# Kernel optimization log

Hardware: AMD Instinct MI355X
Metric: run time of the kernel (lower is better)

Reference implementation:

```python
import jax, jax.numpy as jnp
import numpy as np
from jax import lax

BETA = 1e-07
LAMBDA_TV = 1e-08


def _resize_bilinear_ac(x, out_h, out_w):
    """Bilinear resize with align_corners=True, NCHW layout (matches F.interpolate)."""
    B, C, H, W = x.shape
    ys = jnp.arange(out_h, dtype=jnp.float32) * ((H - 1) / max(out_h - 1, 1))
    xs = jnp.arange(out_w, dtype=jnp.float32) * ((W - 1) / max(out_w - 1, 1))
    y0 = jnp.floor(ys).astype(jnp.int32); y1 = jnp.minimum(y0 + 1, H - 1)
    x0 = jnp.floor(xs).astype(jnp.int32); x1 = jnp.minimum(x0 + 1, W - 1)
    wy = (ys - y0.astype(jnp.float32))[:, None]   # [out_h,1]
    wx = (xs - x0.astype(jnp.float32))[None, :]   # [1,out_w]
    r0 = x[:, :, y0, :]; r1 = x[:, :, y1, :]      # [B,C,out_h,W]
    top = r0[:, :, :, x0] * (1.0 - wx) + r0[:, :, :, x1] * wx
    bot = r1[:, :, :, x0] * (1.0 - wx) + r1[:, :, :, x1] * wx
    return top * (1.0 - wy) + bot * wy


def _levelset_loss(output, target):
    B = output.shape[0]
    # pcentroid computed under no_grad in torch -> stop_gradient here
    num = jnp.einsum('bthw,bchw->btc', target, output)
    den = jnp.sum(output, axis=(2, 3))                       # [B,C]
    pcent = lax.stop_gradient(num / den[:, None, :])          # [B,T,C]
    plevel = target[:, :, None, :, :] - pcent[:, :, :, None, None]  # [B,T,C,H,W]
    return jnp.sum(plevel * plevel * output[:, None]) / B


def _gradient_loss2d(output):
    B = output.shape[0]
    dH = jnp.abs(output[:, :, 1:, :] - output[:, :, :-1, :])
    dW = jnp.abs(output[:, :, :, 1:] - output[:, :, :, :-1])
    return (jnp.sum(dH) + jnp.sum(dW)) / B


def _nonlocal_tv_loss(f_output, f_sem):
    B, Cs, H, W = f_sem.shape
    N = H * W
    fo = _resize_bilinear_ac(f_output, H, W)                  # [B,C,H,W]
    C = fo.shape[1]
    # F.normalize(f_sem, dim=1) (eps=1e-12)
    norm = jnp.sqrt(jnp.sum(f_sem * f_sem, axis=1, keepdims=True))
    sem = f_sem / jnp.maximum(norm, 1e-12)
    sem_f = sem.reshape(B, Cs, N)
    # tau[b,r,p] = relu(<sem_r, sem_p>); normalized by global spatial max per (b,r)
    tau = jax.nn.relu(jnp.einsum('bcr,bcp->brp', sem_f, sem_f))  # [B,N,N]
    tau_max = jnp.max(tau, axis=2, keepdims=True)
    tau_n = tau / (tau_max + 1e-05)
    # torch.matmul(dL[B,C,H,W], tau[B,1,H,W]) summed over everything reduces to
    # sum_{i,k,j} dL[b,c,i,k] * tau[b,k,j] = sum_k (sum_i dL[b,c,i,k]) * (sum_j tau[b,k,j])
    t = tau_n.reshape(B, N, H, W).sum(axis=3)                 # [B,N,H] row-sums of tau
    of = fo.reshape(B, C, N)
    # dL[b,c,r,h,w] = |out_r - out_{(h,w)}| (penalty='l1')
    dL = jnp.abs(of[:, :, :, None, None] - fo[:, :, None, :, :])  # [B,C,N,H,W]
    A = dL.sum(axis=3)                                         # [B,C,N,W] sum over rows i
    return jnp.einsum('bcrk,brk->', A, t) / B


def setup_inputs() -> dict:
    key = jax.random.key(0)
    k1, k2, k3, k4 = jax.random.split(key, 4)
    return {
        'output': jax.random.uniform(k1, (4, 21, 512, 512), dtype=jnp.float32),
        'target': jax.random.uniform(k2, (4, 3, 512, 512), dtype=jnp.float32),
        'f_sem': jax.random.normal(k3, (4, 256, 32, 32), dtype=jnp.float32),
        'f_output': jax.random.uniform(k4, (4, 21, 64, 64), dtype=jnp.float32),
        'use_NonLocal_TV': 1,
    }


def reference(output, target, f_sem, f_output, use_NonLocal_TV):
    loss_LS = _levelset_loss(output, target)
    if use_NonLocal_TV:
        loss_TV = _nonlocal_tv_loss(f_output, f_sem) * LAMBDA_TV
    else:
        loss_TV = _gradient_loss2d(output) * LAMBDA_TV
    loss_MS = (loss_LS + loss_TV) * BETA
    return (loss_LS * BETA, loss_TV * BETA, loss_MS)
```

## Files before the change

kernel.cpp:

```cpp
#include <hip/hip_runtime.h>

#define BETA_F   1e-7f
#define LAMBDA_F 1e-8f

#define HWSZ 262144
#define NBC  84
#define NPIX 1024

#define OFF_FO    0
#define OFF_GSUM  86016
#define OFF_INVN  (86016 + 131072)
#define OFF_RMAX  (217088 + 4096)
#define OFF_LS    (221184 + 4096)
#define OFF_ACC   (225280 + 588)
#define ZERO_START OFF_RMAX
#define ZERO_COUNT (4096 + 588 + 4)

#define N_GRAM_BLK 144

typedef __attribute__((ext_vector_type(8))) short short8;
typedef __attribute__((ext_vector_type(4))) float f32x4;

__device__ const unsigned char RT_[36] =
    {0,0,0,0,0,0,0,0, 1,1,1,1,1,1,1, 2,2,2,2,2,2, 3,3,3,3,3, 4,4,4,4, 5,5,5, 6,6, 7};
__device__ const unsigned char CT_[36] =
    {0,1,2,3,4,5,6,7, 1,2,3,4,5,6,7, 2,3,4,5,6,7, 3,4,5,6,7, 4,5,6,7, 5,6,7, 6,7, 7};

__device__ __forceinline__ unsigned short bf16r(float f) {
    unsigned int u = __float_as_uint(f);
    u += 0x7fffu + ((u >> 16) & 1u);
    return (unsigned short)(u >> 16);
}

__global__ __launch_bounds__(256) void k_prep(const float* __restrict__ fo_in,
                                              const float* __restrict__ fsem,
                                              float* __restrict__ ws) {
    const int bid = blockIdx.x, tid = threadIdx.x;
    if (bid < 19) {
        int i = bid * 256 + tid;
        if (i < ZERO_COUNT) ws[ZERO_START + i] = 0.f;
    } else if (bid < 103) {
        const int bc = bid - 19;
        const float* im = fo_in + bc * 4096;
        for (int p = tid; p < 1024; p += 256) {
            const int oy = p >> 5, ox = p & 31;
            const float R = 63.0f / 31.0f;
            float sy = oy * R, sx = ox * R;
            int y0 = (int)sy, x0 = (int)sx;
            int y1 = min(y0 + 1, 63), x1 = min(x0 + 1, 63);
            float wy = sy - (float)y0, wx = sx - (float)x0;
            float v00 = im[y0 * 64 + x0], v01 = im[y0 * 64 + x1];
            float v10 = im[y1 * 64 + x0], v11 = im[y1 * 64 + x1];
            float top = v00 * (1.f - wx) + v01 * wx;
            float bot = v10 * (1.f - wx) + v11 * wx;
            ws[OFF_FO + bc * NPIX + p] = top * (1.f - wy) + bot * wy;
        }
    } else {
        const int blk = bid - 103;
        const int b = blk >> 4, pg = blk & 15;
        const int p0 = pg * 64;
        const int pi = tid & 63, cg = tid >> 6;
        float s = 0.f;
        for (int c = cg; c < 256; c += 4) {
            float v = fsem[(b * 256 + c) * 1024 + p0 + pi];
            s += v * v;
        }
        __shared__ float red[4][64];
        red[cg][pi] = s;
        __syncthreads();
        if (tid < 64) {
            float t = red[0][tid] + red[1][tid] + red[2][tid] + red[3][tid];
            ws[OFF_INVN + b * 1024 + p0 + tid] = 1.f / fmaxf(sqrtf(t), 1e-12f);
        }
    }
}

__device__ __forceinline__ void acc_px(float4 o, float4 ta, float4 tb, float4 tc,
                                       float& dn, float& n0, float& n1, float& n2,
                                       float& q0, float& q1, float& q2) {
    dn += o.x + o.y + o.z + o.w;
    n0 += ta.x*o.x + ta.y*o.y + ta.z*o.z + ta.w*o.w;
    q0 += ta.x*ta.x*o.x + ta.y*ta.y*o.y + ta.z*ta.z*o.z + ta.w*ta.w*o.w;
    n1 += tb.x*o.x + tb.y*o.y + tb.z*o.z + tb.w*o.w;
    q1 += tb.x*tb.x*o.x + tb.y*tb.y*o.y + tb.z*tb.z*o.z + tb.w*tb.w*o.w;
    n2 += tc.x*o.x + tc.y*o.y + tc.z*o.z + tc.w*o.w;
    q2 += tc.x*tc.x*o.x + tc.y*tc.y*o.y + tc.z*tc.z*o.z + tc.w*tc.w*o.w;
}

#define LSTR 40

__global__ __launch_bounds__(256) void k_main(const float* __restrict__ outp,
                                              const float* __restrict__ tgt,
                                              const float* __restrict__ fsem,
                                              float* __restrict__ ws) {
    __shared__ __align__(16) char smem[20480];
    const int tid = threadIdx.x;

    if (blockIdx.x < N_GRAM_BLK) {
        unsigned short* Asub = (unsigned short*)smem;
        unsigned short* Bsub = (unsigned short*)(smem + 10240);
        const int bid = blockIdx.x;
        const int b = bid / 36, t = bid % 36;
        const int rt = RT_[t], ct = CT_[t];
        const bool diag = (rt == ct);
        const int r0 = rt * 128, c0 = ct * 128;

        const int ch_l = tid & 31, pxg = tid >> 5;
        const int w = tid >> 6, l = tid & 63;
        const int wr = (w >> 1) * 64, wc = (w & 1) * 64;
        const int lr = l & 15, lg = l >> 4;

        f32x4 acc[4][4];
        #pragma unroll
        for (int i = 0; i < 4; ++i)
            #pragma unroll
            for (int j = 0; j < 4; ++j) acc[i][j] = (f32x4){0.f, 0.f, 0.f, 0.f};

        for (int kk = 0; kk < 8; ++kk) {
            __syncthreads();
            const float* fb = fsem + (size_t)(b * 256 + kk * 32 + ch_l) * 1024;
            #pragma unroll
            for (int q = 0; q < 4; ++q) {
                float4 va = *(const float4*)(fb + r0 + pxg * 16 + q * 4);
                float4 vb = *(const float4*)(fb + c0 + pxg * 16 + q * 4);
                const int px = pxg * 16 + q * 4;
                Asub[(px + 0) * LSTR + ch_l] = bf16r(va.x);
                Asub[(px + 1) * LSTR + ch_l] = bf16r(va.y);
                Asub[(px + 2) * LSTR + ch_l] = bf16r(va.z);
                Asub[(px + 3) * LSTR + ch_l] = bf16r(va.w);
                Bsub[(px + 0) * LSTR + ch_l] = bf16r(vb.x);
                Bsub[(px + 1) * LSTR + ch_l] = bf16r(vb.y);
                Bsub[(px + 2) * LSTR + ch_l] = bf16r(vb.z);
                Bsub[(px + 3) * LSTR + ch_l] = bf16r(vb.w);
            }
            __syncthreads();
            short8 a8[4], b8[4];
            #pragma unroll
            for (int fr = 0; fr < 4; ++fr)
                a8[fr] = *(const short8*)(Asub + (wr + fr * 16 + lr) * LSTR + lg * 8);
            #pragma unroll
            for (int fc = 0; fc < 4; ++fc)
                b8[fc] = *(const short8*)(Bsub + (wc + fc * 16 + lr) * LSTR + lg * 8);
            #pragma unroll
            for (int fr = 0; fr < 4; ++fr)
                #pragma unroll
                for (int fc = 0; fc < 4; ++fc)
                    acc[fr][fc] = __builtin_amdgcn_mfma_f32_16x16x32_bf16(
                        a8[fr], b8[fc], acc[fr][fc], 0, 0, 0);
        }

        float ir[4][4], ic[4];
        #pragma unroll
        for (int fr = 0; fr < 4; ++fr)
            #pragma unroll
            for (int rg = 0; rg < 4; ++rg)
                ir[fr][rg] = ws[OFF_INVN + b * 1024 + r0 + wr + fr * 16 + lg * 4 + rg];
        #pragma unroll
        for (int fc = 0; fc < 4; ++fc)
            ic[fc] = ws[OFF_INVN + b * 1024 + c0 + wc + fc * 16 + lr];
        #pragma unroll
        for (int fr = 0; fr < 4; ++fr)
            #pragma unroll
            for (int fc = 0; fc < 4; ++fc)
                #pragma unroll
                for (int rg = 0; rg < 4; ++rg)
                    acc[fr][fc][rg] = fmaxf(acc[fr][fc][rg], 0.f) * ir[fr][rg] * ic[fc];

        #pragma unroll
        for (int fr = 0; fr < 4; ++fr)
            #pragma unroll
            for (int rg = 0; rg < 4; ++rg) {
                float v0 = acc[fr][0][rg] + acc[fr][1][rg];
                float v1 = acc[fr][2][rg] + acc[fr][3][rg];
                float m  = fmaxf(fmaxf(acc[fr][0][rg], acc[fr][1][rg]),
                                 fmaxf(acc[fr][2][rg], acc[fr][3][rg]));
                #pragma unroll
                for (int msk = 1; msk < 16; msk <<= 1) {
                    v0 += __shfl_xor(v0, msk);
                    v1 += __shfl_xor(v1, msk);
                    m = fmaxf(m, __shfl_xor(m, msk));
                }
                if (lr == 0) {
                    const int row = r0 + wr + fr * 16 + lg * 4 + rg;
                    float* g = ws + OFF_GSUM + (size_t)(b * 1024 + row) * 32
                             + ct * 4 + (w & 1) * 2;
                    g[0] = v0; g[1] = v1;
                    atomicMax((int*)&ws[OFF_RMAX + b * 1024 + row], __float_as_int(m));
                }
            }
        if (!diag) {
            #pragma unroll
            for (int fc = 0; fc < 4; ++fc) {
                float c0s = 0.f, c1s = 0.f, cm = 0.f;
                #pragma unroll
                for (int rg = 0; rg < 4; ++rg) {
                    c0s += acc[0][fc][rg] + acc[1][fc][rg];
                    c1s += acc[2][fc][rg] + acc[3][fc][rg];
                    cm = fmaxf(cm, fmaxf(fmaxf(acc[0][fc][rg], acc[1][fc][rg]),
                                         fmaxf(acc[2][fc][rg], acc[3][fc][rg])));
                }
                #pragma unroll
                for (int msk = 16; msk < 64; msk <<= 1) {
                    c0s += __shfl_xor(c0s, msk);
                    c1s += __shfl_xor(c1s, msk);
                    cm = fmaxf(cm, __shfl_xor(cm, msk));
                }
                if (lg == 0) {
                    const int col = c0 + wc + fc * 16 + lr;
                    float* g = ws + OFF_GSUM + (size_t)(b * 1024 + col) * 32
                             + rt * 4 + (w >> 1) * 2;
                    g[0] = c0s; g[1] = c1s;
                    atomicMax((int*)&ws[OFF_RMAX + b * 1024 + col], __float_as_int(cm));
                }
            }
        }
    } else {
        float (*red)[7] = (float (*)[7])smem;
        const int blk = blockIdx.x - N_GRAM_BLK;
        const int slice = blk & 31, bc = blk >> 5;
        const int b = bc / 21;
        const float4* o4 = (const float4*)(outp + (size_t)bc * HWSZ + slice * 8192);
        const float4* t4 = (const float4*)(tgt + (size_t)b * (3 * HWSZ) + slice * 8192);
        float dn = 0, n0 = 0, n1 = 0, n2 = 0, q0 = 0, q1 = 0, q2 = 0;
        #pragma unroll
        for (int half = 0; half < 2; ++half) {
            float4 o[4], ta[4], tb[4], tc[4];
            #pragma unroll
            for (int j = 0; j < 4; ++j) {
                const int i = tid + (half * 4 + j) * 256;
                o[j]  = o4[i];
                ta[j] = t4[i];
                tb[j] = t4[i + 65536];
                tc[j] = t4[i + 131072];
            }
            #pragma unroll
            for (int j = 0; j < 4; ++j)
                acc_px(o[j], ta[j], tb[j], tc[j], dn, n0, n1, n2, q0, q1, q2);
        }
        float vals[7] = {n0, n1, n2, q0, q1, q2, dn};
        #pragma unroll
        for (int j = 0; j < 7; ++j) {
            float v = vals[j];
            #pragma unroll
            for (int off = 32; off; off >>= 1) v += __shfl_xor(v, off);
            if ((tid & 63) == 0) red[tid >> 6][j] = v;
        }
        __syncthreads();
        if (tid < 7) {
            float s = red[0][tid] + red[1][tid] + red[2][tid] + red[3][tid];
            atomicAdd(&ws[OFF_LS + bc * 7 + tid], s);
        }
    }
}

__global__ __launch_bounds__(256) void k_tv(const float* __restrict__ ws,
                                            float* __restrict__ acc_out) {
    const int bc = blockIdx.y;
    const int b = bc / 21;
    const int tid = threadIdx.x;
    __shared__ float4 fo4[256];
    const float4* src = (const float4*)(ws + OFF_FO + bc * NPIX);
    fo4[tid] = src[tid];
    __syncthreads();
    const int r = blockIdx.x * 256 + tid;
    const float v = ((const float*)fo4)[r];
    float ak[32];
    #pragma unroll
    for (int k = 0; k < 32; ++k) ak[k] = 0.f;
    #pragma unroll 4
    for (int h = 0; h < 32; ++h) {
        #pragma unroll
        for (int k4 = 0; k4 < 8; ++k4) {
            float4 f = fo4[h * 8 + k4];
            ak[k4 * 4 + 0] += fabsf(v - f.x);
            ak[k4 * 4 + 1] += fabsf(v - f.y);
            ak[k4 * 4 + 2] += fabsf(v - f.z);
            ak[k4 * 4 + 3] += fabsf(v - f.w);
        }
    }
    const float rm = ws[OFF_RMAX + b * 1024 + r];
    const float inv = 1.f / (rm + 1e-5f);
    const float* t = ws + OFF_GSUM + (b * 1024 + r) * 32;
    float dot = 0.f;
    #pragma unroll
    for (int k = 0; k < 32; ++k) dot += ak[k] * t[k];
    float part = dot * inv;
    #pragma unroll
    for (int off = 32; off; off >>= 1) part += __shfl_xor(part, off);
    __shared__ float red[4];
    if ((tid & 63) == 0) red[tid >> 6] = part;
    __syncthreads();
    if (tid == 0) atomicAdd(acc_out, red[0] + red[1] + red[2] + red[3]);
}

__global__ void k_combine(const float* __restrict__ ws, float* __restrict__ out) {
    const int tid = threadIdx.x;
    float v = 0.f;
    if (tid < NBC) {
        const float* p = ws + OFF_LS + tid * 7;
        float den = p[6];
        v = (p[3] + p[4] + p[5]) - (p[0]*p[0] + p[1]*p[1] + p[2]*p[2]) / den;
    }
    #pragma unroll
    for (int off = 32; off; off >>= 1) v += __shfl_xor(v, off);
    __shared__ float red[2];
    if ((tid & 63) == 0) red[tid >> 6] = v;
    __syncthreads();
    if (tid == 0) {
        float lsv = (red[0] + red[1]) * 0.25f;
        float tvv = ws[OFF_ACC] * 0.25f;
        out[0] = lsv * BETA_F;
        out[1] = tvv * LAMBDA_F * BETA_F;
        out[2] = (lsv + tvv * LAMBDA_F) * BETA_F;
    }
}

extern "C" void kernel_launch(void* const* d_in, const int* in_sizes, int n_in,
                              void* d_out, int out_size, void* d_ws, size_t ws_size,
                              hipStream_t stream) {
    const float* output   = (const float*)d_in[0];
    const float* target   = (const float*)d_in[1];
    const float* f_sem    = (const float*)d_in[2];
    const float* f_output = (const float*)d_in[3];
    float* ws  = (float*)d_ws;
    float* out = (float*)d_out;

    hipLaunchKernelGGL(k_prep,    dim3(167),             dim3(256), 0, stream, f_output, f_sem, ws);
    hipLaunchKernelGGL(k_main,    dim3(N_GRAM_BLK+2688), dim3(256), 0, stream, output, target, f_sem, ws);
    hipLaunchKernelGGL(k_tv,      dim3(4, 84),           dim3(256), 0, stream, ws, ws + OFF_ACC);
    hipLaunchKernelGGL(k_combine, dim3(1),               dim3(128), 0, stream, ws, out);
}
```

Baseline: 198.9 us.

## Reuse target tiles across channels in LDS and load gram fragments directly

The level-set blocks now stage one batch's 3-channel target slice in shared memory and loop over all 21 output channels. Each target value is read from global memory once per batch instead of once per channel. Partial sums are spread over 8 slots per quantity to reduce atomic contention, and the combine kernel sums those slots. The gram tiles drop the LDS transpose and barriers: MFMA fragments are built from strided global loads with packed bf16 conversion, which trades uncoalesced loads for fewer syncs, along with a launch-bounds occupancy hint.

```diff
diff --git a/kernel.cpp b/kernel.cpp
--- a/kernel.cpp
+++ b/kernel.cpp
@@ -12,11 +12,12 @@
 #define OFF_INVN  (86016 + 131072)
 #define OFF_RMAX  (217088 + 4096)
 #define OFF_LS    (221184 + 4096)
-#define OFF_ACC   (225280 + 588)
+#define OFF_ACC   (225280 + 4704)
 #define ZERO_START OFF_RMAX
-#define ZERO_COUNT (4096 + 588 + 4)
+#define ZERO_COUNT (4096 + 4704 + 4)
 
 #define N_GRAM_BLK 144
+#define N_LS_BLK   1024
 
 typedef __attribute__((ext_vector_type(8))) short short8;
 typedef __attribute__((ext_vector_type(4))) float f32x4;
@@ -26,21 +27,28 @@
 __device__ const unsigned char CT_[36] =
     {0,1,2,3,4,5,6,7, 1,2,3,4,5,6,7, 2,3,4,5,6,7, 3,4,5,6,7, 4,5,6,7, 5,6,7, 6,7, 7};
 
-__device__ __forceinline__ unsigned short bf16r(float f) {
-    unsigned int u = __float_as_uint(f);
-    u += 0x7fffu + ((u >> 16) & 1u);
-    return (unsigned short)(u >> 16);
+__device__ __forceinline__ short8 frag8(const float* __restrict__ p) {
+    int u[4];
+    #pragma unroll
+    for (int q = 0; q < 4; ++q) {
+        float lo = p[(2 * q) * 1024];
+        float hi = p[(2 * q + 1) * 1024];
+        asm("v_cvt_pk_bf16_f32 %0, %1, %2" : "=v"(u[q]) : "v"(lo), "v"(hi));
+    }
+    union { int4 i; short8 s; } cvt;
+    cvt.i = make_int4(u[0], u[1], u[2], u[3]);
+    return cvt.s;
 }
 
 __global__ __launch_bounds__(256) void k_prep(const float* __restrict__ fo_in,
                                               const float* __restrict__ fsem,
                                               float* __restrict__ ws) {
     const int bid = blockIdx.x, tid = threadIdx.x;
-    if (bid < 19) {
+    if (bid < 35) {
         int i = bid * 256 + tid;
         if (i < ZERO_COUNT) ws[ZERO_START + i] = 0.f;
-    } else if (bid < 103) {
-        const int bc = bid - 19;
+    } else if (bid < 119) {
+        const int bc = bid - 35;
         const float* im = fo_in + bc * 4096;
         for (int p = tid; p < 1024; p += 256) {
             const int oy = p >> 5, ox = p & 31;
@@ -56,7 +64,7 @@
             ws[OFF_FO + bc * NPIX + p] = top * (1.f - wy) + bot * wy;
         }
     } else {
-        const int blk = bid - 103;
+        const int blk = bid - 119;
         const int b = blk >> 4, pg = blk & 15;
         const int p0 = pg * 64;
         const int pi = tid & 63, cg = tid >> 6;
@@ -87,25 +95,19 @@
     q2 += tc.x*tc.x*o.x + tc.y*tc.y*o.y + tc.z*tc.z*o.z + tc.w*tc.w*o.w;
 }
 
-#define LSTR 40
-
-__global__ __launch_bounds__(256) void k_main(const float* __restrict__ outp,
-                                              const float* __restrict__ tgt,
-                                              const float* __restrict__ fsem,
-                                              float* __restrict__ ws) {
-    __shared__ __align__(16) char smem[20480];
+__global__ __launch_bounds__(256, 4) void k_main(const float* __restrict__ outp,
+                                                 const float* __restrict__ tgt,
+                                                 const float* __restrict__ fsem,
+                                                 float* __restrict__ ws) {
+    __shared__ __align__(16) char smem[12288];
     const int tid = threadIdx.x;
 
     if (blockIdx.x < N_GRAM_BLK) {
-        unsigned short* Asub = (unsigned short*)smem;
-        unsigned short* Bsub = (unsigned short*)(smem + 10240);
         const int bid = blockIdx.x;
         const int b = bid / 36, t = bid % 36;
         const int rt = RT_[t], ct = CT_[t];
         const bool diag = (rt == ct);
         const int r0 = rt * 128, c0 = ct * 128;
-
-        const int ch_l = tid & 31, pxg = tid >> 5;
         const int w = tid >> 6, l = tid & 63;
         const int wr = (w >> 1) * 64, wc = (w & 1) * 64;
         const int lr = l & 15, lg = l >> 4;
@@ -117,30 +119,14 @@
             for (int j = 0; j < 4; ++j) acc[i][j] = (f32x4){0.f, 0.f, 0.f, 0.f};
 
         for (int kk = 0; kk < 8; ++kk) {
-            __syncthreads();
-            const float* fb = fsem + (size_t)(b * 256 + kk * 32 + ch_l) * 1024;
-            #pragma unroll
-            for (int q = 0; q < 4; ++q) {
-                float4 va = *(const float4*)(fb + r0 + pxg * 16 + q * 4);
-                float4 vb = *(const float4*)(fb + c0 + pxg * 16 + q * 4);
-                const int px = pxg * 16 + q * 4;
-                Asub[(px + 0) * LSTR + ch_l] = bf16r(va.x);
-                Asub[(px + 1) * LSTR + ch_l] = bf16r(va.y);
-                Asub[(px + 2) * LSTR + ch_l] = bf16r(va.z);
-                Asub[(px + 3) * LSTR + ch_l] = bf16r(va.w);
-                Bsub[(px + 0) * LSTR + ch_l] = bf16r(vb.x);
-                Bsub[(px + 1) * LSTR + ch_l] = bf16r(vb.y);
-                Bsub[(px + 2) * LSTR + ch_l] = bf16r(vb.z);
-                Bsub[(px + 3) * LSTR + ch_l] = bf16r(vb.w);
-            }
-            __syncthreads();
+            const float* base = fsem + (size_t)(b * 256 + kk * 32 + lg * 8) * 1024;
             short8 a8[4], b8[4];
             #pragma unroll
             for (int fr = 0; fr < 4; ++fr)
-                a8[fr] = *(const short8*)(Asub + (wr + fr * 16 + lr) * LSTR + lg * 8);
+                a8[fr] = frag8(base + r0 + wr + fr * 16 + lr);
             #pragma unroll
             for (int fc = 0; fc < 4; ++fc)
-                b8[fc] = *(const short8*)(Bsub + (wc + fc * 16 + lr) * LSTR + lg * 8);
+                b8[fc] = frag8(base + c0 + wc + fc * 16 + lr);
             #pragma unroll
             for (int fr = 0; fr < 4; ++fr)
                 #pragma unroll
@@ -215,40 +201,45 @@
             }
         }
     } else {
-        float (*red)[7] = (float (*)[7])smem;
+        float* tls = (float*)smem;
         const int blk = blockIdx.x - N_GRAM_BLK;
-        const int slice = blk & 31, bc = blk >> 5;
-        const int b = bc / 21;
-        const float4* o4 = (const float4*)(outp + (size_t)bc * HWSZ + slice * 8192);
-        const float4* t4 = (const float4*)(tgt + (size_t)b * (3 * HWSZ) + slice * 8192);
-        float dn = 0, n0 = 0, n1 = 0, n2 = 0, q0 = 0, q1 = 0, q2 = 0;
-        #pragma unroll
-        for (int half = 0; half < 2; ++half) {
-            float4 o[4], ta[4], tb[4], tc[4];
-            #pragma unroll
-            for (int j = 0; j < 4; ++j) {
-                const int i = tid + (half * 4 + j) * 256;
-                o[j]  = o4[i];
-                ta[j] = t4[i];
-                tb[j] = t4[i + 65536];
-                tc[j] = t4[i + 131072];
+        const int b = blk >> 8, s = blk & 255;
+        const size_t tbase = (size_t)b * (3 * HWSZ) + s * 1024 + tid * 4;
+        #pragma unroll
+        for (int ch = 0; ch < 3; ++ch) {
+            float4 tv = *(const float4*)(tgt + tbase + (size_t)ch * HWSZ);
+            *(float4*)(tls + ch * 1024 + tid * 4) = tv;
+        }
+        __syncthreads();
+        const int w = tid >> 6, lane = tid & 63;
+        for (int c = w; c < 21; c += 4) {
+            const float* obase = outp + (size_t)(b * 21 + c) * HWSZ + s * 1024;
+            float4 o[4], t0[4], t1[4], t2[4];
+            #pragma unroll
+            for (int i = 0; i < 4; ++i)
+                o[i] = *(const float4*)(obase + i * 256 + lane * 4);
+            #pragma unroll
+            for (int i = 0; i < 4; ++i) {
+                const int p = i * 256 + lane * 4;
+                t0[i] = *(const float4*)(tls + p);
+                t1[i] = *(const float4*)(tls + 1024 + p);
+                t2[i] = *(const float4*)(tls + 2048 + p);
             }
-            #pragma unroll
-            for (int j = 0; j < 4; ++j)
-                acc_px(o[j], ta[j], tb[j], tc[j], dn, n0, n1, n2, q0, q1, q2);
-        }
-        float vals[7] = {n0, n1, n2, q0, q1, q2, dn};
-        #pragma unroll
-        for (int j = 0; j < 7; ++j) {
-            float v = vals[j];
-            #pragma unroll
-            for (int off = 32; off; off >>= 1) v += __shfl_xor(v, off);
-            if ((tid & 63) == 0) red[tid >> 6][j] = v;
-        }
-        __syncthreads();
-        if (tid < 7) {
-            float s = red[0][tid] + red[1][tid] + red[2][tid] + red[3][tid];
-            atomicAdd(&ws[OFF_LS + bc * 7 + tid], s);
+            float dn = 0, n0 = 0, n1 = 0, n2 = 0, q0 = 0, q1 = 0, q2 = 0;
+            #pragma unroll
+            for (int i = 0; i < 4; ++i)
+                acc_px(o[i], t0[i], t1[i], t2[i], dn, n0, n1, n2, q0, q1, q2);
+            float vals[7] = {n0, n1, n2, q0, q1, q2, dn};
+            float myv = 0.f;
+            #pragma unroll
+            for (int q = 0; q < 7; ++q) {
+                float v = vals[q];
+                #pragma unroll
+                for (int off = 32; off; off >>= 1) v += __shfl_xor(v, off);
+                if (lane == q) myv = v;
+            }
+            if (lane < 7)
+                atomicAdd(&ws[OFF_LS + (b * 21 + c) * 56 + lane * 8 + (s & 7)], myv);
         }
     }
 }
@@ -297,9 +288,17 @@
     const int tid = threadIdx.x;
     float v = 0.f;
     if (tid < NBC) {
-        const float* p = ws + OFF_LS + tid * 7;
-        float den = p[6];
-        v = (p[3] + p[4] + p[5]) - (p[0]*p[0] + p[1]*p[1] + p[2]*p[2]) / den;
+        const float* p = ws + OFF_LS + tid * 56;
+        float vv[7];
+        #pragma unroll
+        for (int q = 0; q < 7; ++q) {
+            float s = 0.f;
+            #pragma unroll
+            for (int k = 0; k < 8; ++k) s += p[q * 8 + k];
+            vv[q] = s;
+        }
+        float den = vv[6];
+        v = (vv[3] + vv[4] + vv[5]) - (vv[0]*vv[0] + vv[1]*vv[1] + vv[2]*vv[2]) / den;
     }
     #pragma unroll
     for (int off = 32; off; off >>= 1) v += __shfl_xor(v, off);
@@ -325,8 +324,8 @@
     float* ws  = (float*)d_ws;
     float* out = (float*)d_out;
 
-    hipLaunchKernelGGL(k_prep,    dim3(167),             dim3(256), 0, stream, f_output, f_sem, ws);
-    hipLaunchKernelGGL(k_main,    dim3(N_GRAM_BLK+2688), dim3(256), 0, stream, output, target, f_sem, ws);
-    hipLaunchKernelGGL(k_tv,      dim3(4, 84),           dim3(256), 0, stream, ws, ws + OFF_ACC);
-    hipLaunchKernelGGL(k_combine, dim3(1),               dim3(128), 0, stream, ws, out);
-}
+    hipLaunchKernelGGL(k_prep,    dim3(183),                 dim3(256), 0, stream, f_output, f_sem, ws);
+    hipLaunchKernelGGL(k_main,    dim3(N_GRAM_BLK+N_LS_BLK), dim3(256), 0, stream, output, target, f_sem, ws);
+    hipLaunchKernelGGL(k_tv,      dim3(4, 84),               dim3(256), 0, stream, ws, ws + OFF_ACC);
+    hipLaunchKernelGGL(k_combine, dim3(1),                   dim3(128), 0, stream, ws, out);
+}
```

After: 241.7 us. 1.22x slower.
